# Kernel tuning notes

Measured on AMD Instinct MI355X. Metric: run time of the kernel, lower is better.

Reference implementation:

```python
import jax, jax.numpy as jnp
import numpy as np

B, F, D, L, N = 2048, 40, 64, 3, 40  # batch, num_fields, embed_dim, num_layers, num_subspaces


def setup_inputs() -> dict:
    key = jax.random.key(0)
    inputs = jax.random.normal(key, (B, F, D), dtype=jnp.float32)
    # Parameters per layer, matching torch init exactly:
    #   W     = identity(D) repeated over out_subspaces -> [N, D, D]
    #   alpha = ones([num_fields, in_subspaces, out_subspaces]); in_subspaces == F for
    #           layer 0 and == N afterwards; with N == F all layers share shape [F, N, N]
    #   h     = ones([N, D, 1])
    W = jnp.broadcast_to(jnp.eye(D, dtype=jnp.float32), (L, N, D, D)).copy()
    alpha = jnp.ones((L, F, N, N), dtype=jnp.float32)
    h = jnp.ones((L, N, D, 1), dtype=jnp.float32)
    return {"inputs": inputs, "W": W, "alpha": alpha, "h": h}


def _fusion_layer(B0, Bi, W, alpha, h):
    # Original math: fusion[b,n,D,d] = sum_{f,i} alpha[f,i,n] * B0[b,f,D] * Bi[b,i,d]
    #                out[b,n,D]     = sum_d fusion[b,n,D,d] * W[n,D,d] * h[n,d]
    # Reordered to avoid the [b,f,n,D,d] outer-product tensor:
    M = W * h[:, :, 0][:, None, :]                 # [n, D, d] = W * h broadcast over D
    C = jnp.einsum('bid,nDd->binD', Bi, M)         # contract embed dim d first
    out = jnp.einsum('bfD,fin,binD->bnD', B0, alpha, C)
    return out


def reference(inputs, W, alpha, h):
    B_i = inputs
    for l in range(L):
        B_i = _fusion_layer(inputs, B_i, W[l], alpha[l], h[l])
    return B_i
```

## Files before the change

### kernel.cpp

```cpp
#include <hip/hip_runtime.h>


typedef __bf16 bf16x8 __attribute__((ext_vector_type(8)));
typedef float  f32x16 __attribute__((ext_vector_type(16)));
typedef unsigned short us4 __attribute__((ext_vector_type(4)));

constexpr int BATCH = 2048;
constexpr int FDIM  = 40;
constexpr int DDIM  = 64;
constexpr int LAY   = 3;
constexpr int IPAD  = 64;
constexpr int FPAD  = 48;
constexpr int NSPL  = 4;
constexpr int NPB   = FDIM / NSPL;

__device__ __forceinline__ unsigned short f2bf(float f) {
  union { float f; unsigned u; } v; v.f = f;
  unsigned r = v.u + 0x7fff + ((v.u >> 16) & 1);
  return (unsigned short)(r >> 16);
}

__global__ void prep_k(const float* __restrict__ W, const float* __restrict__ h,
                       const float* __restrict__ alpha, const float* __restrict__ inputs,
                       unsigned short* __restrict__ M, unsigned short* __restrict__ AT,
                       unsigned short* __restrict__ B0b, unsigned short* __restrict__ B0T) {
  int j = blockIdx.x * blockDim.x + threadIdx.x;
  const int nM4 = LAY * FDIM * DDIM * DDIM / 4;
  const int nA4 = LAY * FDIM * IPAD * FPAD / 4;
  const int nB4 = BATCH * FDIM * DDIM / 4;
  const int nT4 = BATCH * DDIM * FPAD / 4;
  if (j < nM4) {
    int e  = j * 4;
    int d  = e & 63;
    int ln = e >> 12;
    float4 wv = *reinterpret_cast<const float4*>(W + e);
    float4 hv = *reinterpret_cast<const float4*>(h + ln * DDIM + d);
    us4 o = { f2bf(wv.x * hv.x), f2bf(wv.y * hv.y), f2bf(wv.z * hv.z), f2bf(wv.w * hv.w) };
    *reinterpret_cast<us4*>(M + e) = o;
    return;
  }
  j -= nM4;
  if (j < nA4) {
    int e  = j * 4;
    int f  = e % FPAD;
    int ii = (e / FPAD) % IPAD;
    int n  = (e / (FPAD * IPAD)) % FDIM;
    int l  = e / (FPAD * IPAD * FDIM);
    us4 o = {0, 0, 0, 0};
    if (ii < FDIM) {
#pragma unroll
      for (int k = 0; k < 4; ++k)
        if (f + k < FDIM)
          o[k] = f2bf(alpha[(((size_t)l * FDIM + f + k) * FDIM + ii) * FDIM + n]);
    }
    *reinterpret_cast<us4*>(AT + e) = o;
    return;
  }
  j -= nA4;
  if (j < nB4) {
    int e = j * 4;
    float4 v = *reinterpret_cast<const float4*>(inputs + e);
    us4 o = { f2bf(v.x), f2bf(v.y), f2bf(v.z), f2bf(v.w) };
    *reinterpret_cast<us4*>(B0b + e) = o;
    return;
  }
  j -= nB4;
  if (j >= nT4) return;
  {
    int e  = j * 4;
    int f  = e % FPAD;
    int d  = (e / FPAD) % DDIM;
    int b  = e / (FPAD * DDIM);
    us4 o = {0, 0, 0, 0};
#pragma unroll
    for (int k = 0; k < 4; ++k)
      if (f + k < FDIM)
        o[k] = f2bf(inputs[((size_t)b * FDIM + f + k) * DDIM + d]);
    *reinterpret_cast<us4*>(B0T + e) = o;
  }
}

template <bool FINAL>
__global__ __launch_bounds__(128, 2) void layer_k(
    const unsigned short* __restrict__ Bi,
    const unsigned short* __restrict__ B0T,
    const unsigned short* __restrict__ Mt,
    const unsigned short* __restrict__ ATt,
    void* __restrict__ outp)
{
  const int tid  = threadIdx.x;
  const int lane = tid & 63;
  const int w    = tid >> 6;
  const int c    = lane & 31;
  const int h    = lane >> 5;
  const int bg   = blockIdx.x >> 2;
  const int nBase = (blockIdx.x & 3) * NPB;
  const int bb   = bg * 4 + w * 2;

  bf16x8 aBi[2][2][4];
#pragma unroll
  for (int b2 = 0; b2 < 2; ++b2)
#pragma unroll
    for (int it = 0; it < 2; ++it) {
      int row = it * 32 + c; if (row > FDIM - 1) row = FDIM - 1;
#pragma unroll
      for (int ks = 0; ks < 4; ++ks)
        aBi[b2][it][ks] = *reinterpret_cast<const bf16x8*>(
            Bi + ((size_t)(bb + b2) * FDIM + row) * DDIM + ks * 16 + h * 8);
    }

  bf16x8 bT[2][2][3];
#pragma unroll
  for (int b2 = 0; b2 < 2; ++b2)
#pragma unroll
    for (int dt = 0; dt < 2; ++dt)
#pragma unroll
      for (int ks = 0; ks < 3; ++ks)
        bT[b2][dt][ks] = *reinterpret_cast<const bf16x8*>(
            B0T + ((size_t)(bb + b2) * DDIM + dt * 32 + c) * FPAD + ks * 16 + h * 8);

  for (int ln = 0; ln < NPB; ++ln) {
    const int n = nBase + ln;
    const unsigned short* Mn = Mt  + n * (DDIM * DDIM);
    const unsigned short* An = ATt + n * (IPAD * FPAD);

    bf16x8 mb[2][4];
#pragma unroll
    for (int dt = 0; dt < 2; ++dt)
#pragma unroll
      for (int ks = 0; ks < 4; ++ks)
        mb[dt][ks] = *reinterpret_cast<const bf16x8*>(
            Mn + (dt * 32 + c) * DDIM + ks * 16 + h * 8);

    bf16x8 at[2][3];
#pragma unroll
    for (int it = 0; it < 2; ++it)
#pragma unroll
      for (int ks = 0; ks < 3; ++ks)
        at[it][ks] = *reinterpret_cast<const bf16x8*>(
            An + (it * 32 + c) * FPAD + ks * 16 + h * 8);

    float pout[2][2] = {{0.f, 0.f}, {0.f, 0.f}};

#pragma unroll
    for (int it = 0; it < 2; ++it) {
#pragma unroll
      for (int dt = 0; dt < 2; ++dt) {
        f32x16 aC0 = {0,0,0,0,0,0,0,0,0,0,0,0,0,0,0,0};
        f32x16 aC1 = {0,0,0,0,0,0,0,0,0,0,0,0,0,0,0,0};
        f32x16 aR0 = {0,0,0,0,0,0,0,0,0,0,0,0,0,0,0,0};
        f32x16 aR1 = {0,0,0,0,0,0,0,0,0,0,0,0,0,0,0,0};
#pragma unroll
        for (int ks = 0; ks < 4; ++ks) {
          aC0 = __builtin_amdgcn_mfma_f32_32x32x16_bf16(aBi[0][it][ks], mb[dt][ks], aC0, 0, 0, 0);
          aC1 = __builtin_amdgcn_mfma_f32_32x32x16_bf16(aBi[1][it][ks], mb[dt][ks], aC1, 0, 0, 0);
        }
#pragma unroll
        for (int ks = 0; ks < 3; ++ks) {
          aR0 = __builtin_amdgcn_mfma_f32_32x32x16_bf16(at[it][ks], bT[0][dt][ks], aR0, 0, 0, 0);
          aR1 = __builtin_amdgcn_mfma_f32_32x32x16_bf16(at[it][ks], bT[1][dt][ks], aR1, 0, 0, 0);
        }
        {
          float t0 = 0.f, t1 = 0.f, t2 = 0.f, t3 = 0.f;
#pragma unroll
          for (int r = 0; r < 4; ++r) {
            t0 += aC0[r] * aR0[r];         t1 += aC0[r + 4] * aR0[r + 4];
            t2 += aC0[r + 8] * aR0[r + 8]; t3 += aC0[r + 12] * aR0[r + 12];
          }
          pout[0][dt] += (t0 + t1) + (t2 + t3);
        }
        {
          float t0 = 0.f, t1 = 0.f, t2 = 0.f, t3 = 0.f;
#pragma unroll
          for (int r = 0; r < 4; ++r) {
            t0 += aC1[r] * aR1[r];         t1 += aC1[r + 4] * aR1[r + 4];
            t2 += aC1[r + 8] * aR1[r + 8]; t3 += aC1[r + 12] * aR1[r + 12];
          }
          pout[1][dt] += (t0 + t1) + (t2 + t3);
        }
      }
    }

#pragma unroll
    for (int b2 = 0; b2 < 2; ++b2) {
      float v0 = pout[b2][0] + __shfl_xor(pout[b2][0], 32, 64);
      float v1 = pout[b2][1] + __shfl_xor(pout[b2][1], 32, 64);
      float val = h ? v1 : v0;
      size_t off = ((size_t)(bb + b2) * FDIM + n) * DDIM + lane;
      if (FINAL) ((float*)outp)[off] = val;
      else       ((unsigned short*)outp)[off] = f2bf(val);
    }
  }
}

extern "C" void kernel_launch(void* const* d_in, const int* in_sizes, int n_in,
                              void* d_out, int out_size, void* d_ws, size_t ws_size,
                              hipStream_t stream) {
  const float* inputs = (const float*)d_in[0];
  const float* W      = (const float*)d_in[1];
  const float* alpha  = (const float*)d_in[2];
  const float* h      = (const float*)d_in[3];

  char* ws = (char*)d_ws;
  const size_t S   = (size_t)BATCH * FDIM * DDIM * 2;
  const size_t ST  = (size_t)BATCH * DDIM * FPAD * 2;
  unsigned short* Bi1 = (unsigned short*)(ws);
  unsigned short* Bi2 = (unsigned short*)(ws + S);
  unsigned short* B0b = (unsigned short*)(ws + 2 * S);
  unsigned short* B0T = (unsigned short*)(ws + 3 * S);
  unsigned short* Mb  = (unsigned short*)(ws + 3 * S + ST);
  unsigned short* ATb = (unsigned short*)(ws + 3 * S + ST + (size_t)LAY * FDIM * DDIM * DDIM * 2);

  const int nPrep4 = (LAY * FDIM * DDIM * DDIM + LAY * FDIM * IPAD * FPAD
                    + BATCH * FDIM * DDIM + BATCH * DDIM * FPAD) / 4;
  prep_k<<<(nPrep4 + 255) / 256, 256, 0, stream>>>(W, h, alpha, inputs, Mb, ATb, B0b, B0T);

  dim3 grid(BATCH / 4 * NSPL), blk(128);
  const size_t mL = (size_t)FDIM * DDIM * DDIM;
  const size_t aL = (size_t)FDIM * IPAD * FPAD;
  layer_k<false><<<grid, blk, 0, stream>>>(B0b, B0T, Mb, ATb, Bi1);
  layer_k<false><<<grid, blk, 0, stream>>>(Bi1, B0T, Mb + mL, ATb + aL, Bi2);
  layer_k<true ><<<grid, blk, 0, stream>>>(Bi2, B0T, Mb + 2 * mL, ATb + 2 * aL, d_out);
}
```

Measured before the change: 263.1 us.

## Split input prep into LDS-transposed kernel and double-buffer per-subspace weight loads

Moves the input bf16 conversion and transpose into a separate per-batch kernel that stages rows in shared memory, so B0T reads become coalesced. The layer kernel changes from two batches per wave with 128 threads to one batch per wave with 256 threads, cutting register pressure. It also double-buffers the M and alpha tile loads across subspaces, wraps the MFMA blocks in s_setprio, and uses packed float2 math for the reduction. Per-wave weight reuse drops, since each loaded M and alpha tile now serves one batch instead of two, and issuing one more kernel adds launch overhead.

```diff
diff --git a/kernel.cpp b/kernel.cpp
--- a/kernel.cpp
+++ b/kernel.cpp
@@ -3,6 +3,7 @@
 
 typedef __bf16 bf16x8 __attribute__((ext_vector_type(8)));
 typedef float  f32x16 __attribute__((ext_vector_type(16)));
+typedef float  f32x2  __attribute__((ext_vector_type(2)));
 typedef unsigned short us4 __attribute__((ext_vector_type(4)));
 
 constexpr int BATCH = 2048;
@@ -21,14 +22,11 @@
 }
 
 __global__ void prep_k(const float* __restrict__ W, const float* __restrict__ h,
-                       const float* __restrict__ alpha, const float* __restrict__ inputs,
-                       unsigned short* __restrict__ M, unsigned short* __restrict__ AT,
-                       unsigned short* __restrict__ B0b, unsigned short* __restrict__ B0T) {
+                       const float* __restrict__ alpha,
+                       unsigned short* __restrict__ M, unsigned short* __restrict__ AT) {
   int j = blockIdx.x * blockDim.x + threadIdx.x;
   const int nM4 = LAY * FDIM * DDIM * DDIM / 4;
   const int nA4 = LAY * FDIM * IPAD * FPAD / 4;
-  const int nB4 = BATCH * FDIM * DDIM / 4;
-  const int nT4 = BATCH * DDIM * FPAD / 4;
   if (j < nM4) {
     int e  = j * 4;
     int d  = e & 63;
@@ -40,7 +38,8 @@
     return;
   }
   j -= nM4;
-  if (j < nA4) {
+  if (j >= nA4) return;
+  {
     int e  = j * 4;
     int f  = e % FPAD;
     int ii = (e / FPAD) % IPAD;
@@ -54,34 +53,39 @@
           o[k] = f2bf(alpha[(((size_t)l * FDIM + f + k) * FDIM + ii) * FDIM + n]);
     }
     *reinterpret_cast<us4*>(AT + e) = o;
-    return;
-  }
-  j -= nA4;
-  if (j < nB4) {
-    int e = j * 4;
-    float4 v = *reinterpret_cast<const float4*>(inputs + e);
+  }
+}
+
+__global__ __launch_bounds__(256) void prep_b_k(const float* __restrict__ inputs,
+                                                unsigned short* __restrict__ B0b,
+                                                unsigned short* __restrict__ B0T) {
+  __shared__ float lds[FDIM][DDIM + 1];
+  const int b = blockIdx.x;
+  const float* src = inputs + (size_t)b * FDIM * DDIM;
+  for (int cch = threadIdx.x; cch < FDIM * DDIM / 4; cch += 256) {
+    float4 v = reinterpret_cast<const float4*>(src)[cch];
+    int e = cch * 4;
+    int f = e >> 6, d = e & 63;
+    lds[f][d] = v.x; lds[f][d + 1] = v.y; lds[f][d + 2] = v.z; lds[f][d + 3] = v.w;
     us4 o = { f2bf(v.x), f2bf(v.y), f2bf(v.z), f2bf(v.w) };
-    *reinterpret_cast<us4*>(B0b + e) = o;
-    return;
-  }
-  j -= nB4;
-  if (j >= nT4) return;
-  {
-    int e  = j * 4;
-    int f  = e % FPAD;
-    int d  = (e / FPAD) % DDIM;
-    int b  = e / (FPAD * DDIM);
+    reinterpret_cast<us4*>(B0b + (size_t)b * FDIM * DDIM)[cch] = o;
+  }
+  __syncthreads();
+  for (int cch = threadIdx.x; cch < DDIM * FPAD / 4; cch += 256) {
+    int f4 = cch % (FPAD / 4);
+    int d  = cch / (FPAD / 4);
     us4 o = {0, 0, 0, 0};
-#pragma unroll
-    for (int k = 0; k < 4; ++k)
-      if (f + k < FDIM)
-        o[k] = f2bf(inputs[((size_t)b * FDIM + f + k) * DDIM + d]);
-    *reinterpret_cast<us4*>(B0T + e) = o;
+    if (f4 < FDIM / 4) {
+      int f = f4 * 4;
+      o[0] = f2bf(lds[f][d]);     o[1] = f2bf(lds[f + 1][d]);
+      o[2] = f2bf(lds[f + 2][d]); o[3] = f2bf(lds[f + 3][d]);
+    }
+    reinterpret_cast<us4*>(B0T + (size_t)b * DDIM * FPAD)[cch] = o;
   }
 }
 
 template <bool FINAL>
-__global__ __launch_bounds__(128, 2) void layer_k(
+__global__ __launch_bounds__(256, 2) void layer_k(
     const unsigned short* __restrict__ Bi,
     const unsigned short* __restrict__ B0T,
     const unsigned short* __restrict__ Mt,
@@ -93,104 +97,91 @@
   const int w    = tid >> 6;
   const int c    = lane & 31;
   const int h    = lane >> 5;
-  const int bg   = blockIdx.x >> 2;
   const int nBase = (blockIdx.x & 3) * NPB;
-  const int bb   = bg * 4 + w * 2;
-
-  bf16x8 aBi[2][2][4];
-#pragma unroll
-  for (int b2 = 0; b2 < 2; ++b2)
-#pragma unroll
-    for (int it = 0; it < 2; ++it) {
-      int row = it * 32 + c; if (row > FDIM - 1) row = FDIM - 1;
-#pragma unroll
-      for (int ks = 0; ks < 4; ++ks)
-        aBi[b2][it][ks] = *reinterpret_cast<const bf16x8*>(
-            Bi + ((size_t)(bb + b2) * FDIM + row) * DDIM + ks * 16 + h * 8);
-    }
-
-  bf16x8 bT[2][2][3];
-#pragma unroll
-  for (int b2 = 0; b2 < 2; ++b2)
-#pragma unroll
-    for (int dt = 0; dt < 2; ++dt)
-#pragma unroll
-      for (int ks = 0; ks < 3; ++ks)
-        bT[b2][dt][ks] = *reinterpret_cast<const bf16x8*>(
-            B0T + ((size_t)(bb + b2) * DDIM + dt * 32 + c) * FPAD + ks * 16 + h * 8);
-
-  for (int ln = 0; ln < NPB; ++ln) {
-    const int n = nBase + ln;
+  const int b    = (blockIdx.x >> 2) * 4 + w;
+
+  bf16x8 aBi[2][4];
+#pragma unroll
+  for (int it = 0; it < 2; ++it) {
+    int row = it * 32 + c; if (row > FDIM - 1) row = FDIM - 1;
+#pragma unroll
+    for (int ks = 0; ks < 4; ++ks)
+      aBi[it][ks] = *reinterpret_cast<const bf16x8*>(
+          Bi + ((size_t)b * FDIM + row) * DDIM + ks * 16 + h * 8);
+  }
+
+  bf16x8 bT[2][3];
+#pragma unroll
+  for (int dt = 0; dt < 2; ++dt)
+#pragma unroll
+    for (int ks = 0; ks < 3; ++ks)
+      bT[dt][ks] = *reinterpret_cast<const bf16x8*>(
+          B0T + ((size_t)b * DDIM + dt * 32 + c) * FPAD + ks * 16 + h * 8);
+
+  bf16x8 mbA[2][4], atA[2][3], mbB[2][4], atB[2][3];
+
+  auto loadn = [&](bf16x8 (&mb)[2][4], bf16x8 (&at)[2][3], int n) {
     const unsigned short* Mn = Mt  + n * (DDIM * DDIM);
     const unsigned short* An = ATt + n * (IPAD * FPAD);
-
-    bf16x8 mb[2][4];
 #pragma unroll
     for (int dt = 0; dt < 2; ++dt)
 #pragma unroll
       for (int ks = 0; ks < 4; ++ks)
         mb[dt][ks] = *reinterpret_cast<const bf16x8*>(
             Mn + (dt * 32 + c) * DDIM + ks * 16 + h * 8);
-
-    bf16x8 at[2][3];
 #pragma unroll
     for (int it = 0; it < 2; ++it)
 #pragma unroll
       for (int ks = 0; ks < 3; ++ks)
         at[it][ks] = *reinterpret_cast<const bf16x8*>(
             An + (it * 32 + c) * FPAD + ks * 16 + h * 8);
-
-    float pout[2][2] = {{0.f, 0.f}, {0.f, 0.f}};
-
+  };
+
+  auto compute = [&](const bf16x8 (&mb)[2][4], const bf16x8 (&at)[2][3], int n) {
+    float pout[2] = {0.f, 0.f};
 #pragma unroll
     for (int it = 0; it < 2; ++it) {
 #pragma unroll
       for (int dt = 0; dt < 2; ++dt) {
-        f32x16 aC0 = {0,0,0,0,0,0,0,0,0,0,0,0,0,0,0,0};
-        f32x16 aC1 = {0,0,0,0,0,0,0,0,0,0,0,0,0,0,0,0};
-        f32x16 aR0 = {0,0,0,0,0,0,0,0,0,0,0,0,0,0,0,0};
-        f32x16 aR1 = {0,0,0,0,0,0,0,0,0,0,0,0,0,0,0,0};
-#pragma unroll
-        for (int ks = 0; ks < 4; ++ks) {
-          aC0 = __builtin_amdgcn_mfma_f32_32x32x16_bf16(aBi[0][it][ks], mb[dt][ks], aC0, 0, 0, 0);
-          aC1 = __builtin_amdgcn_mfma_f32_32x32x16_bf16(aBi[1][it][ks], mb[dt][ks], aC1, 0, 0, 0);
+        f32x16 aC = {0,0,0,0,0,0,0,0,0,0,0,0,0,0,0,0};
+        f32x16 aR = {0,0,0,0,0,0,0,0,0,0,0,0,0,0,0,0};
+        __builtin_amdgcn_s_setprio(1);
+#pragma unroll
+        for (int ks = 0; ks < 4; ++ks)
+          aC = __builtin_amdgcn_mfma_f32_32x32x16_bf16(aBi[it][ks], mb[dt][ks], aC, 0, 0, 0);
+#pragma unroll
+        for (int ks = 0; ks < 3; ++ks)
+          aR = __builtin_amdgcn_mfma_f32_32x32x16_bf16(at[it][ks], bT[dt][ks], aR, 0, 0, 0);
+        __builtin_amdgcn_s_setprio(0);
+        f32x2 s0 = {0.f, 0.f}, s1 = {0.f, 0.f};
+#pragma unroll
+        for (int r = 0; r < 4; ++r) {
+          s0 += (f32x2){aC[2 * r],     aC[2 * r + 1]} * (f32x2){aR[2 * r],     aR[2 * r + 1]};
+          s1 += (f32x2){aC[2 * r + 8], aC[2 * r + 9]} * (f32x2){aR[2 * r + 8], aR[2 * r + 9]};
         }
-#pragma unroll
-        for (int ks = 0; ks < 3; ++ks) {
-          aR0 = __builtin_amdgcn_mfma_f32_32x32x16_bf16(at[it][ks], bT[0][dt][ks], aR0, 0, 0, 0);
-          aR1 = __builtin_amdgcn_mfma_f32_32x32x16_bf16(at[it][ks], bT[1][dt][ks], aR1, 0, 0, 0);
-        }
-        {
-          float t0 = 0.f, t1 = 0.f, t2 = 0.f, t3 = 0.f;
-#pragma unroll
-          for (int r = 0; r < 4; ++r) {
-            t0 += aC0[r] * aR0[r];         t1 += aC0[r + 4] * aR0[r + 4];
-            t2 += aC0[r + 8] * aR0[r + 8]; t3 += aC0[r + 12] * aR0[r + 12];
-          }
-          pout[0][dt] += (t0 + t1) + (t2 + t3);
-        }
-        {
-          float t0 = 0.f, t1 = 0.f, t2 = 0.f, t3 = 0.f;
-#pragma unroll
-          for (int r = 0; r < 4; ++r) {
-            t0 += aC1[r] * aR1[r];         t1 += aC1[r + 4] * aR1[r + 4];
-            t2 += aC1[r + 8] * aR1[r + 8]; t3 += aC1[r + 12] * aR1[r + 12];
-          }
-          pout[1][dt] += (t0 + t1) + (t2 + t3);
-        }
+        f32x2 t = s0 + s1;
+        pout[dt] += t.x + t.y;
       }
     }
-
-#pragma unroll
-    for (int b2 = 0; b2 < 2; ++b2) {
-      float v0 = pout[b2][0] + __shfl_xor(pout[b2][0], 32, 64);
-      float v1 = pout[b2][1] + __shfl_xor(pout[b2][1], 32, 64);
-      float val = h ? v1 : v0;
-      size_t off = ((size_t)(bb + b2) * FDIM + n) * DDIM + lane;
-      if (FINAL) ((float*)outp)[off] = val;
-      else       ((unsigned short*)outp)[off] = f2bf(val);
-    }
-  }
+    float v0 = pout[0] + __shfl_xor(pout[0], 32, 64);
+    float v1 = pout[1] + __shfl_xor(pout[1], 32, 64);
+    float val = h ? v1 : v0;
+    size_t off = ((size_t)b * FDIM + n) * DDIM + lane;
+    if (FINAL) ((float*)outp)[off] = val;
+    else       ((unsigned short*)outp)[off] = f2bf(val);
+  };
+
+  loadn(mbA, atA, nBase + 0);
+#pragma unroll 1
+  for (int k = 0; k < NPB - 2; k += 2) {
+    loadn(mbB, atB, nBase + k + 1);
+    compute(mbA, atA, nBase + k);
+    loadn(mbA, atA, nBase + k + 2);
+    compute(mbB, atB, nBase + k + 1);
+  }
+  loadn(mbB, atB, nBase + NPB - 1);
+  compute(mbA, atA, nBase + NPB - 2);
+  compute(mbB, atB, nBase + NPB - 1);
 }
 
 extern "C" void kernel_launch(void* const* d_in, const int* in_sizes, int n_in,
@@ -211,11 +202,11 @@
   unsigned short* Mb  = (unsigned short*)(ws + 3 * S + ST);
   unsigned short* ATb = (unsigned short*)(ws + 3 * S + ST + (size_t)LAY * FDIM * DDIM * DDIM * 2);
 
-  const int nPrep4 = (LAY * FDIM * DDIM * DDIM + LAY * FDIM * IPAD * FPAD
-                    + BATCH * FDIM * DDIM + BATCH * DDIM * FPAD) / 4;
-  prep_k<<<(nPrep4 + 255) / 256, 256, 0, stream>>>(W, h, alpha, inputs, Mb, ATb, B0b, B0T);
-
-  dim3 grid(BATCH / 4 * NSPL), blk(128);
+  prep_b_k<<<BATCH, 256, 0, stream>>>(inputs, B0b, B0T);
+  const int nPrep4 = (LAY * FDIM * DDIM * DDIM + LAY * FDIM * IPAD * FPAD) / 4;
+  prep_k<<<(nPrep4 + 255) / 256, 256, 0, stream>>>(W, h, alpha, Mb, ATb);
+
+  dim3 grid(BATCH / 4 * NSPL), blk(256);
   const size_t mL = (size_t)FDIM * DDIM * DDIM;
   const size_t aL = (size_t)FDIM * IPAD * FPAD;
   layer_k<false><<<grid, blk, 0, stream>>>(B0b, B0T, Mb, ATb, Bi1);
```

Measured after the change: 361.1 us. 37.3% more time.
